# Performance work log

Measured on AMD Instinct MI355X. Metric: run time of the kernel, lower is better.

Reference implementation:

```python
import jax, jax.numpy as jnp
import numpy as np

N, L, H, V = 8192, 512, 64, 50000
NUM_PARENT = 1024


def setup_inputs() -> dict:
    key = jax.random.key(0)
    ks = jax.random.split(key, 12)
    def mat(k, shape):
        return 0.1 * jax.random.normal(k, shape, dtype=jnp.float32)
    return {
        "x_word": jax.random.normal(ks[0], (N, L), dtype=jnp.float32),
        "x_index": jax.random.randint(ks[1], (N, L), 0, V),
        "tree": jax.random.randint(ks[2], (N, 2), 0, N),
        "num_parent": NUM_PARENT,
        "embedding": mat(ks[3], (V, H)),
        "W_z": mat(ks[4], (H, H)),
        "U_z": mat(ks[5], (H, H)),
        "b_z": jnp.zeros((H,), dtype=jnp.float32),
        "W_r": mat(ks[6], (H, H)),
        "U_r": mat(ks[7], (H, H)),
        "b_r": jnp.zeros((H,), dtype=jnp.float32),
        "W_h": mat(ks[8], (H, H)),
        "U_h": mat(ks[9], (H, H)),
        "b_h": jnp.zeros((H,), dtype=jnp.float32),
    }


def _hard_sigmoid(x):
    # torch double-threshold trick == clip(0.2*x + 0.5, 0, 1)
    return jnp.clip(0.2 * x + 0.5, 0.0, 1.0)


def reference(x_word, x_index, tree, num_parent, embedding,
              W_z, U_z, b_z, W_r, U_r, b_r, W_h, U_h, b_h):
    n_nodes = x_word.shape[0]
    hdim = embedding.shape[1]

    def step(node_h, xs):
        word, idx, info = xs  # word: [L] f32, idx: [L] int, info: [2] int
        parent_h = node_h[info[0]]                 # [H]
        child_xe = embedding[idx].T @ word         # [H] weighted embedding sum
        z = _hard_sigmoid(W_z @ child_xe + U_z @ parent_h + b_z)
        r = _hard_sigmoid(W_r @ child_xe + U_r @ parent_h + b_r)
        c = jnp.tanh(W_h @ child_xe + U_h @ (parent_h * r) + b_h)
        h = z * parent_h + (1.0 - z) * c           # [H]
        return node_h.at[info[1]].set(h), h

    node_h0 = jnp.zeros((n_nodes, hdim), dtype=x_word.dtype)
    # original loops i in range(len(x_word) - 1)
    _, child_hs = jax.lax.scan(step, node_h0,
                               (x_word[:-1], x_index[:-1], tree[:-1]))
    # output = max over child_hs[num_parent-1:]
    return jnp.max(child_hs[num_parent - 1:], axis=0)
```

## Files before the change

### kernel.cpp

```cpp
#include <hip/hip_runtime.h>
#include <math.h>

#define NODES  8192
#define STEPS  8191
#define LW     512
#define H      64
#define VOCAB  50000
#define SWEEPK 13

typedef __attribute__((ext_vector_type(2))) float f32x2;

__global__ void ws_too_small_kernel(float* __restrict__ out) {
    if (threadIdx.x < H) out[threadIdx.x] = -12345.0f;
}

__global__ __launch_bounds__(256)
void cvt_emb(const float* __restrict__ emb, unsigned int* __restrict__ embq) {
    int i = blockIdx.x * 256 + threadIdx.x;
    float4 v = reinterpret_cast<const float4*>(emb)[i];
    int w = 0;
    w = __builtin_amdgcn_cvt_pk_fp8_f32(v.x, v.y, w, false);
    w = __builtin_amdgcn_cvt_pk_fp8_f32(v.z, v.w, w, true);
    embq[i] = (unsigned int)w;
}

__global__ __launch_bounds__(256)
void hist_writers(const int* __restrict__ tree, int* __restrict__ count) {
    int j = blockIdx.x * blockDim.x + threadIdx.x;
    if (j < STEPS) atomicAdd(&count[tree[2 * j + 1]], 1);
}

__global__ __launch_bounds__(1024)
void prefix_kernel(const int* __restrict__ cnt, int* __restrict__ off) {
    __shared__ int wsum[16];
    int tid  = threadIdx.x;
    int lane = tid & 63;
    int wv   = tid >> 6;
    int base = tid * 8;

    int v[8], run = 0;
    #pragma unroll
    for (int e = 0; e < 8; ++e) { v[e] = run; run += cnt[base + e]; }

    int x = run;
    #pragma unroll
    for (int d = 1; d < 64; d <<= 1) {
        int y = __shfl_up(x, d, 64);
        if (lane >= d) x += y;
    }
    if (lane == 63) wsum[wv] = x;
    __syncthreads();
    if (wv == 0) {
        int s = (lane < 16) ? wsum[lane] : 0;
        #pragma unroll
        for (int d = 1; d < 16; d <<= 1) {
            int y = __shfl_up(s, d, 64);
            if (lane >= d) s += y;
        }
        if (lane < 16) wsum[lane] = s;
    }
    __syncthreads();
    int wbase = (wv > 0) ? wsum[wv - 1] : 0;
    int tbase = wbase + x - run;
    #pragma unroll
    for (int e = 0; e < 8; ++e) off[base + e] = tbase + v[e];
    if (tid == 1023) off[8192] = tbase + run;
}

__global__ __launch_bounds__(256)
void scatter_writers(const int* __restrict__ tree, const int* __restrict__ woff,
                     int* __restrict__ cursor, int* __restrict__ writers) {
    int j = blockIdx.x * blockDim.x + threadIdx.x;
    if (j >= STEPS) return;
    int v = tree[2 * j + 1];
    int pos = atomicAdd(&cursor[v], 1);
    writers[woff[v] + pos] = j;
}

__global__ __launch_bounds__(256)
void pred_bucket(const int* __restrict__ tree, const int* __restrict__ woff,
                 const int* __restrict__ writers, int* __restrict__ pred) {
    int i = blockIdx.x * blockDim.x + threadIdx.x;
    if (i >= STEPS) return;
    int v  = tree[2 * i];
    int t0 = woff[v], t1 = woff[v + 1];
    int best = -1;
    for (int t = t0; t < t1; ++t) {
        int j = writers[t];
        if (j < i && j > best) best = j;
    }
    pred[i] = best;
}

__global__ __launch_bounds__(1024)
void fused_sched(const int* __restrict__ pred, int* __restrict__ lstart_g,
                 int* __restrict__ order_g) {
    __shared__ int   smem_i[NODES];
    __shared__ short dep[NODES];
    __shared__ int   wsum[16];
    int tid = threadIdx.x;

    short* jmp = (short*)smem_i;
    for (int i = tid; i < NODES; i += 1024) {
        int p = (i < STEPS) ? pred[i] : -1;
        jmp[i] = (short)p;
        dep[i] = (p >= 0) ? 1 : 0;
    }
    __syncthreads();

    for (int r = 0; r < 13; ++r) {
        short nd[8], nj[8];
        #pragma unroll
        for (int e = 0; e < 8; ++e) {
            int i = tid + e * 1024;
            int j = jmp[i];
            if (j >= 0) { nd[e] = (short)(dep[i] + dep[j]); nj[e] = jmp[j]; }
            else        { nd[e] = dep[i];                   nj[e] = -1;     }
        }
        __syncthreads();
        #pragma unroll
        for (int e = 0; e < 8; ++e) {
            int i = tid + e * 1024;
            dep[i] = nd[e];
            jmp[i] = nj[e];
        }
        __syncthreads();
    }

    int d8[8];
    #pragma unroll
    for (int e = 0; e < 8; ++e) d8[e] = dep[tid + e * 1024];
    __syncthreads();

    int* lcnt = smem_i;
    for (int i = tid; i < NODES; i += 1024) lcnt[i] = 0;
    __syncthreads();
    #pragma unroll
    for (int e = 0; e < 8; ++e) {
        int i = tid + e * 1024;
        if (i < STEPS) atomicAdd(&lcnt[d8[e]], 1);
    }
    __syncthreads();

    {
        int lane = tid & 63, wv = tid >> 6, base = tid * 8;
        int v[8], run = 0;
        #pragma unroll
        for (int e = 0; e < 8; ++e) { v[e] = run; run += lcnt[base + e]; }
        int x = run;
        #pragma unroll
        for (int d = 1; d < 64; d <<= 1) {
            int y = __shfl_up(x, d, 64);
            if (lane >= d) x += y;
        }
        if (lane == 63) wsum[wv] = x;
        __syncthreads();
        if (wv == 0) {
            int s = (lane < 16) ? wsum[lane] : 0;
            #pragma unroll
            for (int d = 1; d < 16; d <<= 1) {
                int y = __shfl_up(s, d, 64);
                if (lane >= d) s += y;
            }
            if (lane < 16) wsum[lane] = s;
        }
        __syncthreads();
        int wbase = (wv > 0) ? wsum[wv - 1] : 0;
        int tbase = wbase + x - run;
        #pragma unroll
        for (int e = 0; e < 8; ++e) lstart_g[base + e] = tbase + v[e];
        if (tid == 1023) lstart_g[8192] = tbase + run;
    }
    __threadfence_block();
    __syncthreads();

    for (int i = tid; i < NODES; i += 1024) lcnt[i] = 0;
    __syncthreads();
    #pragma unroll
    for (int e = 0; e < 8; ++e) {
        int i = tid + e * 1024;
        if (i < STEPS) {
            int d = d8[e];
            int pos = atomicAdd(&lcnt[d], 1);
            order_g[lstart_g[d] + pos] = i;
        }
    }
}

__global__ __launch_bounds__(256)
void gather_project(const float* __restrict__ xw, const int* __restrict__ xi,
                    const unsigned int* __restrict__ embq,
                    const float* __restrict__ Wz, const float* __restrict__ Wr,
                    const float* __restrict__ Wh,
                    const float* __restrict__ bz, const float* __restrict__ br,
                    const float* __restrict__ bh,
                    const int* __restrict__ pred,
                    float* __restrict__ A, float* __restrict__ child_h) {
    int i    = blockIdx.x;
    int tid  = threadIdx.x;
    int wave = tid >> 6;
    int lane = tid & 63;
    int g16  = lane >> 2;
    int q4   = lane & 3;

    __shared__ float s_w[LW];
    __shared__ int   s_idx[LW];
    __shared__ float part[4][64];
    __shared__ float xe[64];

    {
        float2 w2 = reinterpret_cast<const float2*>(xw + (size_t)i * LW)[tid];
        int2   i2 = reinterpret_cast<const int2*>(xi + (size_t)i * LW)[tid];
        s_w[2 * tid]     = w2.x;
        s_w[2 * tid + 1] = w2.y;
        s_idx[2 * tid]     = i2.x;
        s_idx[2 * tid + 1] = i2.y;
    }
    __syncthreads();

    const uint4* E = reinterpret_cast<const uint4*>(embq);
    int base_l = wave * 128 + g16;

    float acc[16];
    #pragma unroll
    for (int c = 0; c < 16; ++c) acc[c] = 0.f;

    uint4 q[8];
    float wgt[8];
    #pragma unroll
    for (int u = 0; u < 8; ++u) {
        int l   = base_l + u * 16;
        int idx = s_idx[l];
        wgt[u]  = s_w[l];
        q[u]    = E[(size_t)idx * 4 + q4];
    }
    #pragma unroll
    for (int u = 0; u < 8; ++u) {
        float w = wgt[u];
        unsigned int uw[4] = {q[u].x, q[u].y, q[u].z, q[u].w};
        #pragma unroll
        for (int d = 0; d < 4; ++d) {
            f32x2 lo = __builtin_amdgcn_cvt_pk_f32_fp8((int)uw[d], false);
            f32x2 hi = __builtin_amdgcn_cvt_pk_f32_fp8((int)uw[d], true);
            acc[4 * d + 0] = fmaf(w, lo.x, acc[4 * d + 0]);
            acc[4 * d + 1] = fmaf(w, lo.y, acc[4 * d + 1]);
            acc[4 * d + 2] = fmaf(w, hi.x, acc[4 * d + 2]);
            acc[4 * d + 3] = fmaf(w, hi.y, acc[4 * d + 3]);
        }
    }
    #pragma unroll
    for (int c = 0; c < 16; ++c) {
        acc[c] += __shfl_xor(acc[c], 4,  64);
        acc[c] += __shfl_xor(acc[c], 8,  64);
        acc[c] += __shfl_xor(acc[c], 16, 64);
        acc[c] += __shfl_xor(acc[c], 32, 64);
    }
    if (lane < 4) {
        #pragma unroll
        for (int c = 0; c < 16; ++c) part[wave][lane * 16 + c] = acc[c];
    }
    __syncthreads();
    if (tid < 64) xe[tid] = part[0][tid] + part[1][tid] + part[2][tid] + part[3][tid];
    __syncthreads();

    float s = 0.f;
    if (tid < 192) {
        int o = tid & 63;
        const float* W = (tid < 64) ? Wz : (tid < 128 ? Wr : Wh);
        const float* b = (tid < 64) ? bz : (tid < 128 ? br : bh);
        s = b[o];
        #pragma unroll
        for (int j = 0; j < H; j += 4) {
            float4 w4 = *reinterpret_cast<const float4*>(W + (size_t)o * H + j);
            s = fmaf(w4.x, xe[j],     s);
            s = fmaf(w4.y, xe[j + 1], s);
            s = fmaf(w4.z, xe[j + 2], s);
            s = fmaf(w4.w, xe[j + 3], s);
        }
    }
    bool isroot = (pred[i] < 0);
    if (tid < 64)                part[0][tid]       = s;
    if (tid >= 128 && tid < 192) part[1][tid - 128] = s;
    __syncthreads();
    if (isroot) {
        if (tid < 64) {
            float z = fminf(fmaxf(0.2f * part[0][tid] + 0.5f, 0.f), 1.f);
            float c = tanhf(part[1][tid]);
            child_h[(size_t)i * H + tid] = (1.f - z) * c;
        }
    } else {
        if (tid < 192) A[(size_t)i * 192 + tid] = s;
    }
}

__device__ __forceinline__ void gru_core(
        int i, int lane, const float* __restrict__ A,
        const int* __restrict__ pred,
        const float* uz, const float* ur, const float* uh,
        float* __restrict__ child_h) {
    int p = pred[i];
    float ph = (p >= 0) ? child_h[(size_t)p * H + lane] : 0.f;
    const float* Ai = A + (size_t)i * 192;
    float az = Ai[lane];
    float ar = Ai[64 + lane];
    float ah = Ai[128 + lane];

    #pragma unroll
    for (int j = 0; j < H; ++j) {
        float s = __shfl(ph, j, 64);
        az = fmaf(uz[j], s, az);
        ar = fmaf(ur[j], s, ar);
    }
    float z = fminf(fmaxf(0.2f * az + 0.5f, 0.f), 1.f);
    float r = fminf(fmaxf(0.2f * ar + 0.5f, 0.f), 1.f);
    float phr = ph * r;
    #pragma unroll
    for (int j = 0; j < H; ++j) {
        float s = __shfl(phr, j, 64);
        ah = fmaf(uh[j], s, ah);
    }
    float c = tanhf(ah);
    child_h[(size_t)i * H + lane] = z * ph + (1.f - z) * c;
}

__global__ __launch_bounds__(256)
void sweep_lvl(int k, const int* __restrict__ lstart, const int* __restrict__ order,
               const float* __restrict__ A, const int* __restrict__ pred,
               const float* __restrict__ Uz, const float* __restrict__ Ur,
               const float* __restrict__ Uh, float* __restrict__ child_h) {
    int s0 = lstart[k], s1 = lstart[k + 1];
    int wave = (blockIdx.x * blockDim.x + threadIdx.x) >> 6;
    int lane = threadIdx.x & 63;
    if (s0 + wave >= s1) return;

    float uz[H], ur[H], uh[H];
    #pragma unroll
    for (int j = 0; j < H; j += 4) {
        float4 a4 = *reinterpret_cast<const float4*>(Uz + (size_t)lane * H + j);
        uz[j] = a4.x; uz[j+1] = a4.y; uz[j+2] = a4.z; uz[j+3] = a4.w;
        float4 b4 = *reinterpret_cast<const float4*>(Ur + (size_t)lane * H + j);
        ur[j] = b4.x; ur[j+1] = b4.y; ur[j+2] = b4.z; ur[j+3] = b4.w;
        float4 c4 = *reinterpret_cast<const float4*>(Uh + (size_t)lane * H + j);
        uh[j] = c4.x; uh[j+1] = c4.y; uh[j+2] = c4.z; uh[j+3] = c4.w;
    }
    for (int t = s0 + wave; t < s1; t += 512)
        gru_core(order[t], lane, A, pred, uz, ur, uh, child_h);
}

__global__ __launch_bounds__(1024)
void tail_block(const int* __restrict__ lstart, const int* __restrict__ order,
                const float* __restrict__ A, const int* __restrict__ pred,
                const float* __restrict__ Uz, const float* __restrict__ Ur,
                const float* __restrict__ Uh, float* __restrict__ child_h) {
    int wave = threadIdx.x >> 6;
    int lane = threadIdx.x & 63;
    for (int k = SWEEPK; k < NODES; ++k) {
        int s0 = lstart[k];
        if (s0 >= STEPS) break;
        int s1 = lstart[k + 1];
        for (int t = s0 + wave; t < s1; t += 16) {
            float uz[H], ur[H], uh[H];
            #pragma unroll
            for (int j = 0; j < H; j += 4) {
                float4 a4 = *reinterpret_cast<const float4*>(Uz + (size_t)lane * H + j);
                uz[j] = a4.x; uz[j+1] = a4.y; uz[j+2] = a4.z; uz[j+3] = a4.w;
                float4 b4 = *reinterpret_cast<const float4*>(Ur + (size_t)lane * H + j);
                ur[j] = b4.x; ur[j+1] = b4.y; ur[j+2] = b4.z; ur[j+3] = b4.w;
                float4 c4 = *reinterpret_cast<const float4*>(Uh + (size_t)lane * H + j);
                uh[j] = c4.x; uh[j+1] = c4.y; uh[j+2] = c4.z; uh[j+3] = c4.w;
            }
            gru_core(order[t], lane, A, pred, uz, ur, uh, child_h);
        }
        __syncthreads();
    }
}

__global__ __launch_bounds__(256)
void reduce_partial(const float* __restrict__ child_h,
                    const int* __restrict__ np_ptr,
                    float* __restrict__ partial) {
    int b   = blockIdx.x;
    int tid = threadIdx.x;
    int h   = tid & 63;
    int grp = tid >> 6;
    int np    = *np_ptr;
    int start = np - 1;
    int total = STEPS - start;
    int per   = (total + gridDim.x - 1) / gridDim.x;
    int r0 = start + b * per;
    int r1 = r0 + per; if (r1 > STEPS) r1 = STEPS;
    float m = -INFINITY;
    for (int row = r0 + grp; row < r1; row += 4)
        m = fmaxf(m, child_h[(size_t)row * H + h]);
    __shared__ float sm[4][64];
    sm[grp][h] = m;
    __syncthreads();
    if (tid < 64)
        partial[b * 64 + tid] = fmaxf(fmaxf(sm[0][tid], sm[1][tid]),
                                      fmaxf(sm[2][tid], sm[3][tid]));
}

__global__ void reduce_final(const float* __restrict__ partial,
                             float* __restrict__ out, int nb) {
    int h = threadIdx.x;
    float m = -INFINITY;
    for (int b = 0; b < nb; ++b) m = fmaxf(m, partial[b * 64 + h]);
    out[h] = m;
}

extern "C" void kernel_launch(void* const* d_in, const int* in_sizes, int n_in,
                              void* d_out, int out_size, void* d_ws, size_t ws_size,
                              hipStream_t stream) {
    const float* xw   = (const float*)d_in[0];
    const int*   xi   = (const int*)  d_in[1];
    const int*   tree = (const int*)  d_in[2];
    const int*   np   = (const int*)  d_in[3];
    const float* emb  = (const float*)d_in[4];
    const float* Wz   = (const float*)d_in[5];
    const float* Uz   = (const float*)d_in[6];
    const float* bz   = (const float*)d_in[7];
    const float* Wr   = (const float*)d_in[8];
    const float* Ur   = (const float*)d_in[9];
    const float* br   = (const float*)d_in[10];
    const float* Wh   = (const float*)d_in[11];
    const float* Uh   = (const float*)d_in[12];
    const float* bh   = (const float*)d_in[13];

    size_t bA   = (size_t)STEPS * 192 * 4;
    size_t bCH  = (size_t)STEPS * H   * 4;
    size_t bEH  = (size_t)VOCAB * H   * 1;
    size_t bInt = (size_t)(8192 * 5 + 8256 * 2) * 4;
    size_t bPar = 56 * 64 * 4 + 256;
    size_t need = bA + bCH + bEH + bInt + bPar;
    if (ws_size < need) {
        ws_too_small_kernel<<<1, 64, 0, stream>>>((float*)d_out);
        return;
    }

    char* base = (char*)d_ws;
    float*          A       = (float*)base;                 base += bA;
    float*          child_h = (float*)base;                 base += bCH;
    unsigned int*   embq    = (unsigned int*)base;          base += bEH;
    int*            pred    = (int*)base;
    int*            writers = pred    + 8192;
    int*            order   = writers + 8192;
    int*            count   = order   + 8192;
    int*            cursor  = count   + 8192;
    int*            woff    = cursor  + 8192;
    int*            lstart  = woff    + 8256;
    float*          partial = (float*)(lstart + 8256);

    cvt_emb        <<<3125, 256, 0, stream>>>(emb, embq);

    hipMemsetAsync(count, 0, (size_t)2 * 8192 * sizeof(int), stream);
    hist_writers   <<<32,  256, 0, stream>>>(tree, count);
    prefix_kernel  <<<1,  1024, 0, stream>>>(count, woff);
    scatter_writers<<<32,  256, 0, stream>>>(tree, woff, cursor, writers);
    pred_bucket    <<<32,  256, 0, stream>>>(tree, woff, writers, pred);

    fused_sched    <<<1,  1024, 0, stream>>>(pred, lstart, order);

    gather_project <<<STEPS, 256, 0, stream>>>(xw, xi, embq, Wz, Wr, Wh,
                                               bz, br, bh, pred, A, child_h);

    for (int k = 1; k < SWEEPK; ++k)
        sweep_lvl  <<<128, 256, 0, stream>>>(k, lstart, order, A, pred,
                                             Uz, Ur, Uh, child_h);
    tail_block     <<<1, 1024, 0, stream>>>(lstart, order, A, pred,
                                            Uz, Ur, Uh, child_h);

    reduce_partial <<<56,  256, 0, stream>>>(child_h, np, partial);
    reduce_final   <<<1,    64, 0, stream>>>(partial, (float*)d_out, 56);
}
```

Before: 320.1 us.

## Replace level-by-level sweeps with dataflow recurrence using per-node done flags

Merges the four predecessor-building kernels and the level scheduler into a single one-block schedule kernel that uses shared-memory histograms. It also replaces the per-level sweep launches and the single-block tail with one persistent recurrence kernel. In that kernel each wave spins on a per-node done flag for its parent, then computes and publishes its own flag. This removes many kernel launches and the per-level barriers. The cost is spin-wait polling, fences, and a risk of deadlock if waves processing dependent nodes are not co-resident, which a guard counter bounds.

```diff
diff --git a/kernel.cpp b/kernel.cpp
--- a/kernel.cpp
+++ b/kernel.cpp
@@ -6,7 +6,7 @@
 #define LW     512
 #define H      64
 #define VOCAB  50000
-#define SWEEPK 13
+#define RWAVES 512
 
 typedef __attribute__((ext_vector_type(2))) float f32x2;
 
@@ -24,129 +24,27 @@
     embq[i] = (unsigned int)w;
 }
 
-__global__ __launch_bounds__(256)
-void hist_writers(const int* __restrict__ tree, int* __restrict__ count) {
-    int j = blockIdx.x * blockDim.x + threadIdx.x;
-    if (j < STEPS) atomicAdd(&count[tree[2 * j + 1]], 1);
-}
-
 __global__ __launch_bounds__(1024)
-void prefix_kernel(const int* __restrict__ cnt, int* __restrict__ off) {
+void build_schedule(const int* __restrict__ tree, int* __restrict__ writers_g,
+                    int* __restrict__ pred_g, int* __restrict__ lstart_g,
+                    int* __restrict__ order_g) {
+    __shared__ int s_off[NODES + 8];
     __shared__ int wsum[16];
     int tid  = threadIdx.x;
     int lane = tid & 63;
     int wv   = tid >> 6;
-    int base = tid * 8;
-
-    int v[8], run = 0;
-    #pragma unroll
-    for (int e = 0; e < 8; ++e) { v[e] = run; run += cnt[base + e]; }
-
-    int x = run;
-    #pragma unroll
-    for (int d = 1; d < 64; d <<= 1) {
-        int y = __shfl_up(x, d, 64);
-        if (lane >= d) x += y;
-    }
-    if (lane == 63) wsum[wv] = x;
-    __syncthreads();
-    if (wv == 0) {
-        int s = (lane < 16) ? wsum[lane] : 0;
-        #pragma unroll
-        for (int d = 1; d < 16; d <<= 1) {
-            int y = __shfl_up(s, d, 64);
-            if (lane >= d) s += y;
-        }
-        if (lane < 16) wsum[lane] = s;
-    }
-    __syncthreads();
-    int wbase = (wv > 0) ? wsum[wv - 1] : 0;
-    int tbase = wbase + x - run;
-    #pragma unroll
-    for (int e = 0; e < 8; ++e) off[base + e] = tbase + v[e];
-    if (tid == 1023) off[8192] = tbase + run;
-}
-
-__global__ __launch_bounds__(256)
-void scatter_writers(const int* __restrict__ tree, const int* __restrict__ woff,
-                     int* __restrict__ cursor, int* __restrict__ writers) {
-    int j = blockIdx.x * blockDim.x + threadIdx.x;
-    if (j >= STEPS) return;
-    int v = tree[2 * j + 1];
-    int pos = atomicAdd(&cursor[v], 1);
-    writers[woff[v] + pos] = j;
-}
-
-__global__ __launch_bounds__(256)
-void pred_bucket(const int* __restrict__ tree, const int* __restrict__ woff,
-                 const int* __restrict__ writers, int* __restrict__ pred) {
-    int i = blockIdx.x * blockDim.x + threadIdx.x;
-    if (i >= STEPS) return;
-    int v  = tree[2 * i];
-    int t0 = woff[v], t1 = woff[v + 1];
-    int best = -1;
-    for (int t = t0; t < t1; ++t) {
-        int j = writers[t];
-        if (j < i && j > best) best = j;
-    }
-    pred[i] = best;
-}
-
-__global__ __launch_bounds__(1024)
-void fused_sched(const int* __restrict__ pred, int* __restrict__ lstart_g,
-                 int* __restrict__ order_g) {
-    __shared__ int   smem_i[NODES];
-    __shared__ short dep[NODES];
-    __shared__ int   wsum[16];
-    int tid = threadIdx.x;
-
-    short* jmp = (short*)smem_i;
-    for (int i = tid; i < NODES; i += 1024) {
-        int p = (i < STEPS) ? pred[i] : -1;
-        jmp[i] = (short)p;
-        dep[i] = (p >= 0) ? 1 : 0;
-    }
-    __syncthreads();
-
-    for (int r = 0; r < 13; ++r) {
-        short nd[8], nj[8];
-        #pragma unroll
-        for (int e = 0; e < 8; ++e) {
-            int i = tid + e * 1024;
-            int j = jmp[i];
-            if (j >= 0) { nd[e] = (short)(dep[i] + dep[j]); nj[e] = jmp[j]; }
-            else        { nd[e] = dep[i];                   nj[e] = -1;     }
-        }
-        __syncthreads();
-        #pragma unroll
-        for (int e = 0; e < 8; ++e) {
-            int i = tid + e * 1024;
-            dep[i] = nd[e];
-            jmp[i] = nj[e];
-        }
-        __syncthreads();
-    }
-
-    int d8[8];
-    #pragma unroll
-    for (int e = 0; e < 8; ++e) d8[e] = dep[tid + e * 1024];
-    __syncthreads();
-
-    int* lcnt = smem_i;
-    for (int i = tid; i < NODES; i += 1024) lcnt[i] = 0;
-    __syncthreads();
-    #pragma unroll
-    for (int e = 0; e < 8; ++e) {
-        int i = tid + e * 1024;
-        if (i < STEPS) atomicAdd(&lcnt[d8[e]], 1);
-    }
+
+    for (int i = tid; i < NODES + 8; i += 1024) s_off[i] = 0;
+    __syncthreads();
+    for (int j = tid; j < STEPS; j += 1024)
+        atomicAdd(&s_off[tree[2 * j + 1]], 1);
     __syncthreads();
 
     {
-        int lane = tid & 63, wv = tid >> 6, base = tid * 8;
+        int base = tid * 8;
         int v[8], run = 0;
         #pragma unroll
-        for (int e = 0; e < 8; ++e) { v[e] = run; run += lcnt[base + e]; }
+        for (int e = 0; e < 8; ++e) { v[e] = run; run += s_off[base + e]; }
         int x = run;
         #pragma unroll
         for (int d = 1; d < 64; d <<= 1) {
@@ -168,6 +66,105 @@
         int wbase = (wv > 0) ? wsum[wv - 1] : 0;
         int tbase = wbase + x - run;
         #pragma unroll
+        for (int e = 0; e < 8; ++e) s_off[base + e] = tbase + v[e];
+    }
+    __syncthreads();
+
+    for (int j = tid; j < STEPS; j += 1024) {
+        int v = tree[2 * j + 1];
+        int pos = atomicAdd(&s_off[v], 1);
+        writers_g[pos] = j;
+    }
+    __syncthreads();
+
+    int pr[8];
+    #pragma unroll
+    for (int e = 0; e < 8; ++e) {
+        int i = tid + e * 1024;
+        int best = -1;
+        if (i < STEPS) {
+            int v  = tree[2 * i];
+            int t1 = s_off[v];
+            int t0 = (v > 0) ? s_off[v - 1] : 0;
+            for (int t = t0; t < t1; ++t) {
+                int j = writers_g[t];
+                if (j < i && j > best) best = j;
+            }
+            pred_g[i] = best;
+        }
+        pr[e] = best;
+    }
+    __syncthreads();
+
+    short* jmp = (short*)s_off;
+    short* dep = (short*)s_off + NODES;
+    #pragma unroll
+    for (int e = 0; e < 8; ++e) {
+        int i = tid + e * 1024;
+        jmp[i] = (short)pr[e];
+        dep[i] = (pr[e] >= 0) ? 1 : 0;
+    }
+    __syncthreads();
+
+    for (int r = 0; r < 13; ++r) {
+        short nd[8], nj[8];
+        #pragma unroll
+        for (int e = 0; e < 8; ++e) {
+            int i = tid + e * 1024;
+            int j = jmp[i];
+            if (j >= 0) { nd[e] = (short)(dep[i] + dep[j]); nj[e] = jmp[j]; }
+            else        { nd[e] = dep[i];                   nj[e] = -1;     }
+        }
+        __syncthreads();
+        #pragma unroll
+        for (int e = 0; e < 8; ++e) {
+            int i = tid + e * 1024;
+            dep[i] = nd[e];
+            jmp[i] = nj[e];
+        }
+        __syncthreads();
+    }
+
+    int d8[8];
+    #pragma unroll
+    for (int e = 0; e < 8; ++e) d8[e] = dep[tid + e * 1024];
+    __syncthreads();
+
+    int* lcnt = s_off;
+    for (int i = tid; i < NODES; i += 1024) lcnt[i] = 0;
+    __syncthreads();
+    #pragma unroll
+    for (int e = 0; e < 8; ++e) {
+        int i = tid + e * 1024;
+        if (i < STEPS) atomicAdd(&lcnt[d8[e]], 1);
+    }
+    __syncthreads();
+    {
+        int base = tid * 8;
+        int v[8], run = 0;
+        #pragma unroll
+        for (int e = 0; e < 8; ++e) { v[e] = run; run += lcnt[base + e]; }
+        int x = run;
+        #pragma unroll
+        for (int d = 1; d < 64; d <<= 1) {
+            int y = __shfl_up(x, d, 64);
+            if (lane >= d) x += y;
+        }
+        if (lane == 63) wsum[wv] = x;
+        __syncthreads();
+        if (wv == 0) {
+            int s = (lane < 16) ? wsum[lane] : 0;
+            #pragma unroll
+            for (int d = 1; d < 16; d <<= 1) {
+                int y = __shfl_up(s, d, 64);
+                if (lane >= d) s += y;
+            }
+            if (lane < 16) wsum[lane] = s;
+        }
+        __syncthreads();
+        int wbase = (wv > 0) ? wsum[wv - 1] : 0;
+        int tbase = wbase + x - run;
+        #pragma unroll
         for (int e = 0; e < 8; ++e) lstart_g[base + e] = tbase + v[e];
         if (tid == 1023) lstart_g[8192] = tbase + run;
     }
@@ -195,7 +192,8 @@
                     const float* __restrict__ bz, const float* __restrict__ br,
                     const float* __restrict__ bh,
                     const int* __restrict__ pred,
-                    float* __restrict__ A, float* __restrict__ child_h) {
+                    float* __restrict__ A, float* __restrict__ child_h,
+                    int* __restrict__ done) {
     int i    = blockIdx.x;
     int tid  = threadIdx.x;
     int wave = tid >> 6;
@@ -279,6 +277,7 @@
         }
     }
     bool isroot = (pred[i] < 0);
+    if (tid == 0) done[i] = isroot ? 1 : 0;
     if (tid < 64)                part[0][tid]       = s;
     if (tid >= 128 && tid < 192) part[1][tid - 128] = s;
     __syncthreads();
@@ -293,45 +292,16 @@
     }
 }
 
-__device__ __forceinline__ void gru_core(
-        int i, int lane, const float* __restrict__ A,
-        const int* __restrict__ pred,
-        const float* uz, const float* ur, const float* uh,
-        float* __restrict__ child_h) {
-    int p = pred[i];
-    float ph = (p >= 0) ? child_h[(size_t)p * H + lane] : 0.f;
-    const float* Ai = A + (size_t)i * 192;
-    float az = Ai[lane];
-    float ar = Ai[64 + lane];
-    float ah = Ai[128 + lane];
-
-    #pragma unroll
-    for (int j = 0; j < H; ++j) {
-        float s = __shfl(ph, j, 64);
-        az = fmaf(uz[j], s, az);
-        ar = fmaf(ur[j], s, ar);
-    }
-    float z = fminf(fmaxf(0.2f * az + 0.5f, 0.f), 1.f);
-    float r = fminf(fmaxf(0.2f * ar + 0.5f, 0.f), 1.f);
-    float phr = ph * r;
-    #pragma unroll
-    for (int j = 0; j < H; ++j) {
-        float s = __shfl(phr, j, 64);
-        ah = fmaf(uh[j], s, ah);
-    }
-    float c = tanhf(ah);
-    child_h[(size_t)i * H + lane] = z * ph + (1.f - z) * c;
-}
-
 __global__ __launch_bounds__(256)
-void sweep_lvl(int k, const int* __restrict__ lstart, const int* __restrict__ order,
-               const float* __restrict__ A, const int* __restrict__ pred,
-               const float* __restrict__ Uz, const float* __restrict__ Ur,
-               const float* __restrict__ Uh, float* __restrict__ child_h) {
-    int s0 = lstart[k], s1 = lstart[k + 1];
-    int wave = (blockIdx.x * blockDim.x + threadIdx.x) >> 6;
+void recurrence(const int* __restrict__ lstart, const int* __restrict__ order,
+                const float* __restrict__ A, const int* __restrict__ pred,
+                const float* __restrict__ Uz, const float* __restrict__ Ur,
+                const float* __restrict__ Uh, float* __restrict__ child_h,
+                int* __restrict__ done) {
+    int gw   = (blockIdx.x * blockDim.x + threadIdx.x) >> 6;
     int lane = threadIdx.x & 63;
-    if (s0 + wave >= s1) return;
+    int t0   = lstart[1];
+    if (t0 + gw >= STEPS) return;
 
     float uz[H], ur[H], uh[H];
     #pragma unroll
@@ -343,35 +313,44 @@
         float4 c4 = *reinterpret_cast<const float4*>(Uh + (size_t)lane * H + j);
         uh[j] = c4.x; uh[j+1] = c4.y; uh[j+2] = c4.z; uh[j+3] = c4.w;
     }
-    for (int t = s0 + wave; t < s1; t += 512)
-        gru_core(order[t], lane, A, pred, uz, ur, uh, child_h);
-}
-
-__global__ __launch_bounds__(1024)
-void tail_block(const int* __restrict__ lstart, const int* __restrict__ order,
-                const float* __restrict__ A, const int* __restrict__ pred,
-                const float* __restrict__ Uz, const float* __restrict__ Ur,
-                const float* __restrict__ Uh, float* __restrict__ child_h) {
-    int wave = threadIdx.x >> 6;
-    int lane = threadIdx.x & 63;
-    for (int k = SWEEPK; k < NODES; ++k) {
-        int s0 = lstart[k];
-        if (s0 >= STEPS) break;
-        int s1 = lstart[k + 1];
-        for (int t = s0 + wave; t < s1; t += 16) {
-            float uz[H], ur[H], uh[H];
-            #pragma unroll
-            for (int j = 0; j < H; j += 4) {
-                float4 a4 = *reinterpret_cast<const float4*>(Uz + (size_t)lane * H + j);
-                uz[j] = a4.x; uz[j+1] = a4.y; uz[j+2] = a4.z; uz[j+3] = a4.w;
-                float4 b4 = *reinterpret_cast<const float4*>(Ur + (size_t)lane * H + j);
-                ur[j] = b4.x; ur[j+1] = b4.y; ur[j+2] = b4.z; ur[j+3] = b4.w;
-                float4 c4 = *reinterpret_cast<const float4*>(Uh + (size_t)lane * H + j);
-                uh[j] = c4.x; uh[j+1] = c4.y; uh[j+2] = c4.z; uh[j+3] = c4.w;
-            }
-            gru_core(order[t], lane, A, pred, uz, ur, uh, child_h);
-        }
-        __syncthreads();
+
+    for (int t = t0 + gw; t < STEPS; t += RWAVES) {
+        int i = order[t];
+        int p = pred[i];
+        const float* Ai = A + (size_t)i * 192;
+        float az = Ai[lane];
+        float ar = Ai[64 + lane];
+        float ah = Ai[128 + lane];
+
+        int guard = 0;
+        while (__hip_atomic_load(done + p, __ATOMIC_RELAXED,
+                                 __HIP_MEMORY_SCOPE_AGENT) == 0) {
+            __builtin_amdgcn_s_sleep(1);
+            if (++guard > (1 << 22)) break;
+        }
+        __threadfence();
+
+        float ph = child_h[(size_t)p * H + lane];
+        #pragma unroll
+        for (int j = 0; j < H; ++j) {
+            float s = __shfl(ph, j, 64);
+            az = fmaf(uz[j], s, az);
+            ar = fmaf(ur[j], s, ar);
+        }
+        float z = fminf(fmaxf(0.2f * az + 0.5f, 0.f), 1.f);
+        float r = fminf(fmaxf(0.2f * ar + 0.5f, 0.f), 1.f);
+        float phr = ph * r;
+        #pragma unroll
+        for (int j = 0; j < H; ++j) {
+            float s = __shfl(phr, j, 64);
+            ah = fmaf(uh[j], s, ah);
+        }
+        float c = tanhf(ah);
+        child_h[(size_t)i * H + lane] = z * ph + (1.f - z) * c;
+        __threadfence();
+        if (lane == 0)
+            __hip_atomic_store(done + i, 1, __ATOMIC_RELAXED,
+                               __HIP_MEMORY_SCOPE_AGENT);
     }
 }
 
@@ -429,7 +408,7 @@
     size_t bA   = (size_t)STEPS * 192 * 4;
     size_t bCH  = (size_t)STEPS * H   * 4;
     size_t bEH  = (size_t)VOCAB * H   * 1;
-    size_t bInt = (size_t)(8192 * 5 + 8256 * 2) * 4;
+    size_t bInt = (size_t)(8192 * 4 + 8256) * 4;
     size_t bPar = 56 * 64 * 4 + 256;
     size_t need = bA + bCH + bEH + bInt + bPar;
     if (ws_size < need) {
@@ -444,30 +423,20 @@
     int*            pred    = (int*)base;
     int*            writers = pred    + 8192;
     int*            order   = writers + 8192;
-    int*            count   = order   + 8192;
-    int*            cursor  = count   + 8192;
-    int*            woff    = cursor  + 8192;
-    int*            lstart  = woff    + 8256;
+    int*            done    = order   + 8192;
+    int*            lstart  = done    + 8192;
     float*          partial = (float*)(lstart + 8256);
 
     cvt_emb        <<<3125, 256, 0, stream>>>(emb, embq);
 
-    hipMemsetAsync(count, 0, (size_t)2 * 8192 * sizeof(int), stream);
-    hist_writers   <<<32,  256, 0, stream>>>(tree, count);
-    prefix_kernel  <<<1,  1024, 0, stream>>>(count, woff);
-    scatter_writers<<<32,  256, 0, stream>>>(tree, woff, cursor, writers);
-    pred_bucket    <<<32,  256, 0, stream>>>(tree, woff, writers, pred);
-
-    fused_sched    <<<1,  1024, 0, stream>>>(pred, lstart, order);
+    build_schedule <<<1,  1024, 0, stream>>>(tree, writers, pred, lstart, order);
 
     gather_project <<<STEPS, 256, 0, stream>>>(xw, xi, embq, Wz, Wr, Wh,
-                                               bz, br, bh, pred, A, child_h);
-
-    for (int k = 1; k < SWEEPK; ++k)
-        sweep_lvl  <<<128, 256, 0, stream>>>(k, lstart, order, A, pred,
-                                             Uz, Ur, Uh, child_h);
-    tail_block     <<<1, 1024, 0, stream>>>(lstart, order, A, pred,
-                                            Uz, Ur, Uh, child_h);
+                                               bz, br, bh, pred, A, child_h,
+                                               done);
+
+    recurrence     <<<128, 256, 0, stream>>>(lstart, order, A, pred,
+                                             Uz, Ur, Uh, child_h, done);
 
     reduce_partial <<<56,  256, 0, stream>>>(child_h, np, partial);
     reduce_final   <<<1,    64, 0, stream>>>(partial, (float*)d_out, 56);
```

Measured after the change: 344.9 us. 7.7% more time.
